# Kernel tuning notes

Hardware: AMD Instinct MI355X
Metric: run time of the kernel (lower is better)

The kernel has to match this reference:

```python
import jax, jax.numpy as jnp
import numpy as np
from jax import lax

NUM_AGNN_LAYERS = 32  # module stacks hidden_dim AGNNConv layers
EPS = 1e-12           # F.normalize clamp


def setup_inputs() -> dict:
    key = jax.random.key(0)
    k1, k2, k3, k4 = jax.random.split(key, 4)
    N, F_in, H, C, E = 100000, 512, 32, 40, 3200000
    x = jax.random.normal(k1, (N, F_in), dtype=jnp.float32)
    edge_index = jax.random.randint(k2, (2, E), 0, N, dtype=jnp.int64)
    W1 = jax.random.normal(k3, (F_in, H), dtype=jnp.float32) * (1.0 / np.sqrt(F_in))
    b1 = jnp.zeros((H,), dtype=jnp.float32)
    W2 = jax.random.normal(k4, (H, C), dtype=jnp.float32) * (1.0 / np.sqrt(H))
    b2 = jnp.zeros((C,), dtype=jnp.float32)
    return {"x": x, "edge_index": edge_index, "W1": W1, "b1": b1, "W2": W2, "b2": b2}


def reference(x, edge_index, W1, b1, W2, b2):
    N = x.shape[0]
    loops = jnp.arange(N, dtype=edge_index.dtype)
    src = jnp.concatenate([edge_index[0], loops])  # message source j
    dst = jnp.concatenate([edge_index[1], loops])  # message target i (softmax group)

    def agnn(h, _):
        # cosine attention, beta = 1 (requires_grad=False)
        norm = jnp.maximum(jnp.linalg.norm(h, axis=-1, keepdims=True), EPS)
        hn = h / norm
        alpha = jnp.sum(hn[src] * hn[dst], axis=-1)               # [E+N]
        m = jax.ops.segment_max(alpha, dst, num_segments=N)       # stable softmax
        e = jnp.exp(alpha - m[dst])
        s = jax.ops.segment_sum(e, dst, num_segments=N)
        coef = e / s[dst]
        out = jax.ops.segment_sum(h[src] * coef[:, None], dst, num_segments=N)
        return out, None

    h = jax.nn.relu(x @ W1 + b1)
    h, _ = lax.scan(agnn, h, None, length=NUM_AGNN_LAYERS)
    logits = h @ W2 + b2
    return jax.nn.log_softmax(logits, axis=1)
```

## Files before the change

kernel.cpp:

```cpp
#include <hip/hip_runtime.h>
#include <math.h>


#define HDIM 32
#define NBMAX 1024
#define BSH 7
#define CHUNK 32768
#define TXP 36
#define TWP 36

typedef _Float16 f16;
typedef _Float16 v2h __attribute__((ext_vector_type(2)));

struct __attribute__((aligned(16))) H8 { v2h p[4]; };
struct __attribute__((aligned(8)))  H4 { v2h p[2]; };

#if defined(__has_builtin)
#if __has_builtin(__builtin_amdgcn_fdot2)
#define FDOT2(a, b, c) __builtin_amdgcn_fdot2((a), (b), (c), false)
#endif
#if __has_builtin(__builtin_amdgcn_update_dpp)
#define HAS_DPP 1
#endif
#endif
#ifndef FDOT2
#define FDOT2(a, b, c) fmaf((float)(a)[1], (float)(b)[1], fmaf((float)(a)[0], (float)(b)[0], (c)))
#endif

static __device__ __forceinline__ float quad_sum(float x) {
#ifdef HAS_DPP
    x += __int_as_float(__builtin_amdgcn_update_dpp(
        0, __float_as_int(x), 0xB1 , 0xF, 0xF, true));
    x += __int_as_float(__builtin_amdgcn_update_dpp(
        0, __float_as_int(x), 0x4E , 0xF, 0xF, true));
#else
    x += __shfl_xor(x, 1);
    x += __shfl_xor(x, 2);
#endif
    return x;
}

static __device__ __forceinline__ int eread(const int* __restrict__ e, int i64, long long idx) {
    return i64 ? e[2 * idx] : e[idx];
}

__global__ void k_flag(const int* __restrict__ e, int* __restrict__ flag) {
    if (blockIdx.x == 0 && threadIdx.x == 0) {
        int z = 0;
        for (int k = 0; k < 64; ++k) z |= e[2 * k + 1];
        *flag = (z == 0) ? 1 : 0;
    }
}

__global__ void k_zero(int* __restrict__ p, int n) {
    int i = blockIdx.x * blockDim.x + threadIdx.x;
    if (i < n) p[i] = 0;
}

__launch_bounds__(256) __global__
void k_hist(const int* __restrict__ e, const int* __restrict__ flag,
            int* __restrict__ gc, int* __restrict__ blockOffs,
            long long E, long long M) {
    __shared__ int bh[NBMAX];
    for (int t = threadIdx.x; t < NBMAX; t += 256) bh[t] = 0;
    __syncthreads();
    int i64 = *flag;
    long long base = (long long)blockIdx.x * CHUNK;
    long long end = base + CHUNK < M ? base + CHUNK : M;
    for (long long m = base + threadIdx.x; m < end; m += 256) {
        int d = (m < E) ? eread(e, i64, E + m) : (int)(m - E);
        atomicAdd(&bh[d >> BSH], 1);
    }
    __syncthreads();
    for (int t = threadIdx.x; t < NBMAX; t += 256) {
        int c = bh[t];
        int off = 0;
        if (c) off = atomicAdd(&gc[t], c);
        blockOffs[(size_t)blockIdx.x * NBMAX + t] = off;
    }
}

__launch_bounds__(256) __global__
void k_bscan(const int* __restrict__ gc, int* __restrict__ bbase,
             int* __restrict__ rp, int N) {
    __shared__ int lds[256];
    int t = threadIdx.x;
    int v[4];
#pragma unroll
    for (int d = 0; d < 4; ++d) v[d] = gc[t * 4 + d];
    int tsum = v[0] + v[1] + v[2] + v[3];
    lds[t] = tsum;
    __syncthreads();
    int acc = tsum;
    for (int sh = 1; sh < 256; sh <<= 1) {
        int x = (t >= sh) ? lds[t - sh] : 0;
        __syncthreads();
        acc += x;
        lds[t] = acc;
        __syncthreads();
    }
    if (t == 255) { rp[N] = acc; bbase[NBMAX] = acc; }
    int run = acc - tsum;
#pragma unroll
    for (int d = 0; d < 4; ++d) { bbase[t * 4 + d] = run; run += v[d]; }
}

__launch_bounds__(256) __global__
void k_part(const int* __restrict__ e, const int* __restrict__ flag,
            const int* __restrict__ bbase, const int* __restrict__ blockOffs,
            int2* __restrict__ pair, long long E, long long M) {
    __shared__ int cur[NBMAX];
    for (int t = threadIdx.x; t < NBMAX; t += 256)
        cur[t] = bbase[t] + blockOffs[(size_t)blockIdx.x * NBMAX + t];
    __syncthreads();
    int i64 = *flag;
    long long base = (long long)blockIdx.x * CHUNK;
    long long end = base + CHUNK < M ? base + CHUNK : M;
    for (long long m = base + threadIdx.x; m < end; m += 256) {
        int s, d;
        if (m < E) { s = eread(e, i64, m); d = eread(e, i64, E + m); }
        else { s = d = (int)(m - E); }
        int pos = atomicAdd(&cur[d >> BSH], 1);
        pair[pos] = make_int2(s, d);
    }
}

__launch_bounds__(256) __global__
void k_fine(const int2* __restrict__ pair, const int* __restrict__ bbase,
            int* __restrict__ rp, int* __restrict__ col, int N) {
    __shared__ int cnt[128];
    __shared__ int sc[128];
    int b = blockIdx.x;
    int beg = bbase[b];
    int end = bbase[b + 1];
    int t = threadIdx.x;
    if (t < 128) cnt[t] = 0;
    __syncthreads();
    for (int k = beg + t; k < end; k += 256)
        atomicAdd(&cnt[pair[k].y & 127], 1);
    __syncthreads();
    if (t < 128) sc[t] = cnt[t];
    __syncthreads();
    for (int sh = 1; sh < 128; sh <<= 1) {
        int x = 0;
        if (t < 128 && t >= sh) x = sc[t - sh];
        __syncthreads();
        if (t < 128) sc[t] += x;
        __syncthreads();
    }
    if (t < 128) {
        int basepos = beg + sc[t] - cnt[t];
        int d = (b << BSH) + t;
        if (d < N) rp[d] = basepos;
        cnt[t] = basepos;
    }
    __syncthreads();
    for (int k = beg + t; k < end; k += 256) {
        int2 p = pair[k];
        int pos = atomicAdd(&cnt[p.y & 127], 1);
        col[pos] = p.x;
    }
}

__launch_bounds__(256, 4) __global__
void k_gemm1(const float* __restrict__ x, const float* __restrict__ W1,
             const float* __restrict__ b1, f16* __restrict__ h, int N) {
    __shared__ float xt[2][128 * TXP];
    __shared__ float wt[2][32 * TWP];
    int tid = threadIdx.x;
    int cg = tid & 7;
    int ty = tid >> 3;
    int rbase = blockIdx.x * 128;
    float4 bias = *(const float4*)(b1 + 4 * cg);
    float acc[4][4];
#pragma unroll
    for (int m = 0; m < 4; ++m) {
        acc[m][0] = bias.x; acc[m][1] = bias.y;
        acc[m][2] = bias.z; acc[m][3] = bias.w;
    }
    int xrow = tid >> 3;
    int xkin = tid & 7;
    float4 gx[4];
    float4 gw;
    {
        int kc = 0;
#pragma unroll
        for (int j = 0; j < 4; ++j) {
            int slot = tid + j * 256;
            int row = slot >> 3, kin = slot & 7;
            int r = rbase + row;
            gx[j] = (r < N) ? *(const float4*)(x + (size_t)r * 512 + kc * 32 + kin * 4)
                            : make_float4(0.f, 0.f, 0.f, 0.f);
        }
        int wrow = tid >> 3, wkin = tid & 7;
        gw = *(const float4*)(W1 + (size_t)(kc * 32 + wrow) * 32 + wkin * 4);
#pragma unroll
        for (int j = 0; j < 4; ++j) {
            int slot = tid + j * 256;
            int row = slot >> 3, kin = slot & 7;
            *(float4*)(&xt[0][row * TXP + kin * 4]) = gx[j];
        }
        *(float4*)(&wt[0][wrow * TWP + wkin * 4]) = gw;
    }
    __syncthreads();
    for (int kc = 0; kc < 16; ++kc) {
        int buf = kc & 1;
        if (kc + 1 < 16) {
            int kn = kc + 1;
#pragma unroll
            for (int j = 0; j < 4; ++j) {
                int slot = tid + j * 256;
                int row = slot >> 3, kin = slot & 7;
                int r = rbase + row;
                gx[j] = (r < N) ? *(const float4*)(x + (size_t)r * 512 + kn * 32 + kin * 4)
                                : make_float4(0.f, 0.f, 0.f, 0.f);
            }
            gw = *(const float4*)(W1 + (size_t)(kn * 32 + (tid >> 3)) * 32 + (tid & 7) * 4);
        }
        const float* xb = xt[buf];
        const float* wb = wt[buf];
#pragma unroll
        for (int k4 = 0; k4 < 8; ++k4) {
            float4 w0 = *(const float4*)(wb + (k4 * 4 + 0) * TWP + 4 * cg);
            float4 w1 = *(const float4*)(wb + (k4 * 4 + 1) * TWP + 4 * cg);
            float4 w2 = *(const float4*)(wb + (k4 * 4 + 2) * TWP + 4 * cg);
            float4 w3 = *(const float4*)(wb + (k4 * 4 + 3) * TWP + 4 * cg);
#pragma unroll
            for (int m = 0; m < 4; ++m) {
                float4 xv = *(const float4*)(xb + (ty + 32 * m) * TXP + k4 * 4);
                acc[m][0] = fmaf(xv.x, w0.x, acc[m][0]);
                acc[m][1] = fmaf(xv.x, w0.y, acc[m][1]);
                acc[m][2] = fmaf(xv.x, w0.z, acc[m][2]);
                acc[m][3] = fmaf(xv.x, w0.w, acc[m][3]);
                acc[m][0] = fmaf(xv.y, w1.x, acc[m][0]);
                acc[m][1] = fmaf(xv.y, w1.y, acc[m][1]);
                acc[m][2] = fmaf(xv.y, w1.z, acc[m][2]);
                acc[m][3] = fmaf(xv.y, w1.w, acc[m][3]);
                acc[m][0] = fmaf(xv.z, w2.x, acc[m][0]);
                acc[m][1] = fmaf(xv.z, w2.y, acc[m][1]);
                acc[m][2] = fmaf(xv.z, w2.z, acc[m][2]);
                acc[m][3] = fmaf(xv.z, w2.w, acc[m][3]);
                acc[m][0] = fmaf(xv.w, w3.x, acc[m][0]);
                acc[m][1] = fmaf(xv.w, w3.y, acc[m][1]);
                acc[m][2] = fmaf(xv.w, w3.z, acc[m][2]);
                acc[m][3] = fmaf(xv.w, w3.w, acc[m][3]);
            }
        }
        if (kc + 1 < 16) {
            int nbuf = buf ^ 1;
#pragma unroll
            for (int j = 0; j < 4; ++j) {
                int slot = tid + j * 256;
                int row = slot >> 3, kin = slot & 7;
                *(float4*)(&xt[nbuf][row * TXP + kin * 4]) = gx[j];
            }
            *(float4*)(&wt[nbuf][(tid >> 3) * TWP + (tid & 7) * 4]) = gw;
            __syncthreads();
        }
    }
    (void)xrow; (void)xkin;
#pragma unroll
    for (int m = 0; m < 4; ++m) {
        int r = rbase + ty + 32 * m;
        if (r < N) {
            H4 o;
            o.p[0][0] = (f16)fmaxf(acc[m][0], 0.0f);
            o.p[0][1] = (f16)fmaxf(acc[m][1], 0.0f);
            o.p[1][0] = (f16)fmaxf(acc[m][2], 0.0f);
            o.p[1][1] = (f16)fmaxf(acc[m][3], 0.0f);
            *(H4*)(h + (size_t)r * HDIM + 4 * cg) = o;
        }
    }
}

__launch_bounds__(256) __global__
void k_agnn(const f16* __restrict__ h_in, f16* __restrict__ h_out,
            const int* __restrict__ rp, const int* __restrict__ col, int N) {
    int wave = threadIdx.x >> 6;
    int lane = threadIdx.x & 63;
    int i = blockIdx.x * 4 + wave;
    if (i >= N) return;
    int beg = rp[i];
    int deg = rp[i + 1] - beg;
    int eloc = lane >> 2;
    int c8 = lane & 3;
    H8 hi = *(const H8*)(h_in + (size_t)i * HDIM + 8 * c8);
    float dsi = 0.0f;
#pragma unroll
    for (int j = 0; j < 4; ++j) dsi = FDOT2(hi.p[j], hi.p[j], dsi);
    dsi = quad_sum(dsi);
    float inv_i = 1.0f / fmaxf(sqrtf(dsi), 1e-12f);
    float s_run = 0.0f;
    float acc[8] = {0.f, 0.f, 0.f, 0.f, 0.f, 0.f, 0.f, 0.f};
    int nchunk = (deg + 15) >> 4;
    int cv = (lane < deg) ? col[beg + lane] : 0;
    H8 rA, rB;
    bool vA, vB = false;
    {
        vA = eloc < deg;
        int s = __shfl(cv, eloc);
        s = vA ? s : 0;
        rA = *(const H8*)(h_in + (size_t)s * HDIM + 8 * c8);
    }
    if (nchunk > 1) {
        int idx = 16 + eloc;
        vB = idx < deg;
        int s = __shfl(cv, 16 | eloc);
        s = vB ? s : 0;
        rB = *(const H8*)(h_in + (size_t)s * HDIM + 8 * c8);
    } else {
        rB = hi;
    }
    for (int ck = 0; ck < nchunk; ++ck) {
        H8 rc = rA;
        bool vc = vA;
        rA = rB; vA = vB;
        int nc = ck + 2;
        if (nc < nchunk) {
            if ((nc & 3) == 0) {
                int idx64 = nc * 16 + lane;
                cv = (idx64 < deg) ? col[beg + idx64] : 0;
            }
            int idx = nc * 16 + eloc;
            vB = idx < deg;
            int s = __shfl(cv, ((nc & 3) << 4) | eloc);
            s = vB ? s : 0;
            rB = *(const H8*)(h_in + (size_t)s * HDIM + 8 * c8);
        }
        float dot = 0.0f, dsj = 0.0f;
#pragma unroll
        for (int j = 0; j < 4; ++j) {
            dot = FDOT2(rc.p[j], hi.p[j], dot);
            dsj = FDOT2(rc.p[j], rc.p[j], dsj);
        }
        dot = quad_sum(dot);
        dsj = quad_sum(dsj);
        float inv_j = 1.0f / fmaxf(sqrtf(dsj), 1e-12f);
        float e = vc ? __expf(fmaf(dot, inv_i * inv_j, -1.0f)) : 0.0f;
        s_run += e;
#pragma unroll
        for (int j = 0; j < 4; ++j) {
            acc[2 * j + 0] = fmaf(e, (float)rc.p[j][0], acc[2 * j + 0]);
            acc[2 * j + 1] = fmaf(e, (float)rc.p[j][1], acc[2 * j + 1]);
        }
    }
    float s_tot = s_run;
#pragma unroll
    for (int mask = 4; mask <= 32; mask <<= 1) s_tot += __shfl_xor(s_tot, mask);
#pragma unroll
    for (int mask = 4; mask <= 32; mask <<= 1) {
#pragma unroll
        for (int j = 0; j < 8; ++j) acc[j] += __shfl_xor(acc[j], mask);
    }
    float invs = 1.0f / s_tot;
#pragma unroll
    for (int j = 0; j < 8; ++j) acc[j] *= invs;
    if (lane < 4) {
        H8 o;
#pragma unroll
        for (int j = 0; j < 4; ++j) {
            o.p[j][0] = (f16)acc[2 * j + 0];
            o.p[j][1] = (f16)acc[2 * j + 1];
        }
        *(H8*)(h_out + (size_t)i * HDIM + 8 * lane) = o;
    }
}

__launch_bounds__(256) __global__
void k_gemm2(const f16* __restrict__ h, const float* __restrict__ W2,
             const float* __restrict__ b2, float* __restrict__ out, int N) {
    int wave = threadIdx.x >> 6;
    int lane = threadIdx.x & 63;
    int i = blockIdx.x * 4 + wave;
    if (i >= N) return;
    bool act = lane < 40;
    float acc = act ? b2[lane] : 0.0f;
    const f16* hr = h + (size_t)i * HDIM;
#pragma unroll
    for (int k = 0; k < HDIM; ++k) {
        float hk = (float)hr[k];
        float w = act ? W2[k * 40 + lane] : 0.0f;
        acc = fmaf(hk, w, acc);
    }
    float logit = act ? acc : -INFINITY;
    float m = logit;
#pragma unroll
    for (int mask = 32; mask >= 1; mask >>= 1) m = fmaxf(m, __shfl_xor(m, mask));
    float e = act ? __expf(logit - m) : 0.0f;
    float s = e;
#pragma unroll
    for (int mask = 32; mask >= 1; mask >>= 1) s += __shfl_xor(s, mask);
    float res = logit - m - __logf(s);
    if (act) out[(size_t)i * 40 + lane] = res;
}

extern "C" void kernel_launch(void* const* d_in, const int* in_sizes, int n_in,
                              void* d_out, int out_size, void* d_ws, size_t ws_size,
                              hipStream_t stream) {
    const float* x  = (const float*)d_in[0];
    const int*   e  = (const int*)d_in[1];
    const float* W1 = (const float*)d_in[2];
    const float* b1 = (const float*)d_in[3];
    const float* W2 = (const float*)d_in[4];
    const float* b2 = (const float*)d_in[5];
    float* out = (float*)d_out;

    const long long E = (long long)in_sizes[1] / 2;
    const int N = in_sizes[0] / 512;
    const long long M = E + N;
    const int nblk = (int)((M + CHUNK - 1) / CHUNK);

    char* w = (char*)d_ws;
    auto alloc = [&](size_t bytes) -> void* {
        void* p = (void*)w;
        w += (bytes + 255) & ~(size_t)255;
        return p;
    };
    int*  flag      = (int*)alloc(4);
    int*  gc        = (int*)alloc(NBMAX * 4);
    int*  bbase     = (int*)alloc((NBMAX + 1) * 4);
    int*  blockOffs = (int*)alloc((size_t)nblk * NBMAX * 4);
    int2* pair      = (int2*)alloc((size_t)M * 8);
    int*  rp        = (int*)alloc(((size_t)N + 1) * 4);
    int*  col       = (int*)alloc((size_t)M * 4);
    f16*  hA   = (f16*)alloc((size_t)N * HDIM * 2);
    f16*  hB   = (f16*)alloc((size_t)N * HDIM * 2);
    if ((size_t)(w - (char*)d_ws) > ws_size) return;

    k_flag<<<1, 64, 0, stream>>>(e, flag);
    k_zero<<<(NBMAX + 255) / 256, 256, 0, stream>>>(gc, NBMAX);
    k_hist<<<nblk, 256, 0, stream>>>(e, flag, gc, blockOffs, E, M);
    k_bscan<<<1, 256, 0, stream>>>(gc, bbase, rp, N);
    k_part<<<nblk, 256, 0, stream>>>(e, flag, bbase, blockOffs, pair, E, M);
    k_fine<<<NBMAX, 256, 0, stream>>>(pair, bbase, rp, col, N);

    k_gemm1<<<(N + 127) / 128, 256, 0, stream>>>(x, W1, b1, hA, N);

    f16 *hin = hA, *hout = hB;
    for (int l = 0; l < 32; ++l) {
        k_agnn<<<(N + 3) / 4, 256, 0, stream>>>(hin, hout, rp, col, N);
        f16* t = hin; hin = hout; hout = t;
    }
    k_gemm2<<<(N + 3) / 4, 256, 0, stream>>>(hin, W2, b2, out, N);
}
```

Before: 2.231 ms.

## Precompute per-node inverse norms in producer kernels and deepen gather prefetch to four chunks

Each producer kernel (gemm1 and every AGNN layer) now writes a per-node inverse L2 norm next to the fp16 features. This removes the per-edge norm computation (an extra dot product, a quad reduction and a sqrt/reciprocal) from the AGNN inner loop, at the cost of one extra 4-byte gather per edge. The neighbour loop is also restructured so four chunks of column indices and rows are loaded ahead instead of two, raising memory-level parallelism. Norms are now computed from fp32 values before the fp16 rounding, so they differ slightly from norms of the stored fp16 features.

Result: no change. 2.256 ms (+1.1%).

```diff
diff --git a/kernel.cpp b/kernel.cpp
--- a/kernel.cpp
+++ b/kernel.cpp
@@ -164,7 +164,8 @@
 
 __launch_bounds__(256, 4) __global__
 void k_gemm1(const float* __restrict__ x, const float* __restrict__ W1,
-             const float* __restrict__ b1, f16* __restrict__ h, int N) {
+             const float* __restrict__ b1, f16* __restrict__ h,
+             float* __restrict__ invn, int N) {
     __shared__ float xt[2][128 * TXP];
     __shared__ float wt[2][32 * TWP];
     int tid = threadIdx.x;
@@ -178,8 +179,6 @@
         acc[m][0] = bias.x; acc[m][1] = bias.y;
         acc[m][2] = bias.z; acc[m][3] = bias.w;
     }
-    int xrow = tid >> 3;
-    int xkin = tid & 7;
     float4 gx[4];
     float4 gw;
     {
@@ -258,23 +257,32 @@
             __syncthreads();
         }
     }
-    (void)xrow; (void)xkin;
 #pragma unroll
     for (int m = 0; m < 4; ++m) {
         int r = rbase + ty + 32 * m;
+        float hv[4];
+        float ss = 0.0f;
+#pragma unroll
+        for (int j = 0; j < 4; ++j) {
+            hv[j] = fmaxf(acc[m][j], 0.0f);
+            ss = fmaf(hv[j], hv[j], ss);
+        }
+        ss += __shfl_xor(ss, 1);
+        ss += __shfl_xor(ss, 2);
+        ss += __shfl_xor(ss, 4);
         if (r < N) {
             H4 o;
-            o.p[0][0] = (f16)fmaxf(acc[m][0], 0.0f);
-            o.p[0][1] = (f16)fmaxf(acc[m][1], 0.0f);
-            o.p[1][0] = (f16)fmaxf(acc[m][2], 0.0f);
-            o.p[1][1] = (f16)fmaxf(acc[m][3], 0.0f);
+            o.p[0][0] = (f16)hv[0]; o.p[0][1] = (f16)hv[1];
+            o.p[1][0] = (f16)hv[2]; o.p[1][1] = (f16)hv[3];
             *(H4*)(h + (size_t)r * HDIM + 4 * cg) = o;
-        }
-    }
-}
-
-__launch_bounds__(256) __global__
-void k_agnn(const f16* __restrict__ h_in, f16* __restrict__ h_out,
+            if (cg == 0) invn[r] = 1.0f / fmaxf(sqrtf(ss), 1e-12f);
+        }
+    }
+}
+
+__launch_bounds__(256) __global__
+void k_agnn(const f16* __restrict__ h_in, const float* __restrict__ inv_in,
+            f16* __restrict__ h_out, float* __restrict__ inv_out,
             const int* __restrict__ rp, const int* __restrict__ col, int N) {
     int wave = threadIdx.x >> 6;
     int lane = threadIdx.x & 63;
@@ -284,66 +292,68 @@
     int deg = rp[i + 1] - beg;
     int eloc = lane >> 2;
     int c8 = lane & 3;
+    float inv_i = inv_in[i];
     H8 hi = *(const H8*)(h_in + (size_t)i * HDIM + 8 * c8);
-    float dsi = 0.0f;
-#pragma unroll
-    for (int j = 0; j < 4; ++j) dsi = FDOT2(hi.p[j], hi.p[j], dsi);
-    dsi = quad_sum(dsi);
-    float inv_i = 1.0f / fmaxf(sqrtf(dsi), 1e-12f);
     float s_run = 0.0f;
     float acc[8] = {0.f, 0.f, 0.f, 0.f, 0.f, 0.f, 0.f, 0.f};
     int nchunk = (deg + 15) >> 4;
-    int cv = (lane < deg) ? col[beg + lane] : 0;
-    H8 rA, rB;
-    bool vA, vB = false;
-    {
-        vA = eloc < deg;
-        int s = __shfl(cv, eloc);
-        s = vA ? s : 0;
-        rA = *(const H8*)(h_in + (size_t)s * HDIM + 8 * c8);
-    }
-    if (nchunk > 1) {
-        int idx = 16 + eloc;
-        vB = idx < deg;
-        int s = __shfl(cv, 16 | eloc);
-        s = vB ? s : 0;
-        rB = *(const H8*)(h_in + (size_t)s * HDIM + 8 * c8);
-    } else {
-        rB = hi;
-    }
-    for (int ck = 0; ck < nchunk; ++ck) {
-        H8 rc = rA;
-        bool vc = vA;
-        rA = rB; vA = vB;
-        int nc = ck + 2;
-        if (nc < nchunk) {
-            if ((nc & 3) == 0) {
-                int idx64 = nc * 16 + lane;
-                cv = (idx64 < deg) ? col[beg + idx64] : 0;
-            }
-            int idx = nc * 16 + eloc;
-            vB = idx < deg;
-            int s = __shfl(cv, ((nc & 3) << 4) | eloc);
-            s = vB ? s : 0;
-            rB = *(const H8*)(h_in + (size_t)s * HDIM + 8 * c8);
-        }
-        float dot = 0.0f, dsj = 0.0f;
-#pragma unroll
-        for (int j = 0; j < 4; ++j) {
-            dot = FDOT2(rc.p[j], hi.p[j], dot);
-            dsj = FDOT2(rc.p[j], rc.p[j], dsj);
-        }
-        dot = quad_sum(dot);
-        dsj = quad_sum(dsj);
-        float inv_j = 1.0f / fmaxf(sqrtf(dsj), 1e-12f);
-        float e = vc ? __expf(fmaf(dot, inv_i * inv_j, -1.0f)) : 0.0f;
-        s_run += e;
-#pragma unroll
-        for (int j = 0; j < 4; ++j) {
-            acc[2 * j + 0] = fmaf(e, (float)rc.p[j][0], acc[2 * j + 0]);
-            acc[2 * j + 1] = fmaf(e, (float)rc.p[j][1], acc[2 * j + 1]);
-        }
-    }
+
+#define CLOADK(k) ((16 * (k) + eloc) < deg ? col[beg + 16 * (k) + eloc] : 0)
+#define RLOAD(Rv, iv, s) do { \
+        Rv = *(const H8*)(h_in + (size_t)(s) * HDIM + 8 * c8); \
+        iv = inv_in[(s)]; \
+    } while (0)
+#define PROC(Rv, iv, vf) do { \
+        float dot_ = 0.0f; \
+        _Pragma("unroll") \
+        for (int j_ = 0; j_ < 4; ++j_) dot_ = FDOT2(Rv.p[j_], hi.p[j_], dot_); \
+        dot_ = quad_sum(dot_); \
+        float e_ = (vf) ? __expf(fmaf(dot_, inv_i * (iv), -1.0f)) : 0.0f; \
+        s_run += e_; \
+        _Pragma("unroll") \
+        for (int j_ = 0; j_ < 4; ++j_) { \
+            acc[2 * j_ + 0] = fmaf(e_, (float)Rv.p[j_][0], acc[2 * j_ + 0]); \
+            acc[2 * j_ + 1] = fmaf(e_, (float)Rv.p[j_][1], acc[2 * j_ + 1]); \
+        } \
+    } while (0)
+
+    int c0 = CLOADK(0), c1 = CLOADK(1), c2 = CLOADK(2), c3 = CLOADK(3);
+    bool v0 = (eloc) < deg;
+    bool v1 = (16 + eloc) < deg;
+    bool v2 = (32 + eloc) < deg;
+    bool v3 = (48 + eloc) < deg;
+    H8 R0, R1, R2, R3;
+    float i0, i1, i2, i3;
+    RLOAD(R0, i0, c0);
+    RLOAD(R1, i1, c1);
+    RLOAD(R2, i2, c2);
+    RLOAD(R3, i3, c3);
+    int n0 = 0, n1 = 0, n2 = 0, n3 = 0;
+    if (nchunk > 4) { n0 = CLOADK(4); n1 = CLOADK(5); n2 = CLOADK(6); n3 = CLOADK(7); }
+
+    int g = 0;
+    if (nchunk > 4) {
+        while (true) {
+            PROC(R0, i0, v0); v0 = (16 * (g + 4) + eloc) < deg; RLOAD(R0, i0, n0);
+            PROC(R1, i1, v1); v1 = (16 * (g + 5) + eloc) < deg; RLOAD(R1, i1, n1);
+            PROC(R2, i2, v2); v2 = (16 * (g + 6) + eloc) < deg; RLOAD(R2, i2, n2);
+            PROC(R3, i3, v3); v3 = (16 * (g + 7) + eloc) < deg; RLOAD(R3, i3, n3);
+            g += 4;
+            if (g + 4 >= nchunk) break;
+            n0 = CLOADK(g + 4); n1 = CLOADK(g + 5);
+            n2 = CLOADK(g + 6); n3 = CLOADK(g + 7);
+        }
+    }
+    int rem = nchunk - g;
+    PROC(R0, i0, v0);
+    if (rem > 1) PROC(R1, i1, v1);
+    if (rem > 2) PROC(R2, i2, v2);
+    if (rem > 3) PROC(R3, i3, v3);
+
+#undef CLOADK
+#undef RLOAD
+#undef PROC
+
     float s_tot = s_run;
 #pragma unroll
     for (int mask = 4; mask <= 32; mask <<= 1) s_tot += __shfl_xor(s_tot, mask);
@@ -353,8 +363,13 @@
         for (int j = 0; j < 8; ++j) acc[j] += __shfl_xor(acc[j], mask);
     }
     float invs = 1.0f / s_tot;
-#pragma unroll
-    for (int j = 0; j < 8; ++j) acc[j] *= invs;
+    float ss = 0.0f;
+#pragma unroll
+    for (int j = 0; j < 8; ++j) {
+        acc[j] *= invs;
+        ss = fmaf(acc[j], acc[j], ss);
+    }
+    ss = quad_sum(ss);
     if (lane < 4) {
         H8 o;
 #pragma unroll
@@ -363,6 +378,7 @@
             o.p[j][1] = (f16)acc[2 * j + 1];
         }
         *(H8*)(h_out + (size_t)i * HDIM + 8 * lane) = o;
+        if (lane == 0) inv_out[i] = 1.0f / fmaxf(sqrtf(ss), 1e-12f);
     }
 }
 
@@ -425,6 +441,8 @@
     int*  col       = (int*)alloc((size_t)M * 4);
     f16*  hA   = (f16*)alloc((size_t)N * HDIM * 2);
     f16*  hB   = (f16*)alloc((size_t)N * HDIM * 2);
+    float* invA = (float*)alloc((size_t)N * 4);
+    float* invB = (float*)alloc((size_t)N * 4);
     if ((size_t)(w - (char*)d_ws) > ws_size) return;
 
     k_flag<<<1, 64, 0, stream>>>(e, flag);
@@ -434,12 +452,14 @@
     k_part<<<nblk, 256, 0, stream>>>(e, flag, bbase, blockOffs, pair, E, M);
     k_fine<<<NBMAX, 256, 0, stream>>>(pair, bbase, rp, col, N);
 
-    k_gemm1<<<(N + 127) / 128, 256, 0, stream>>>(x, W1, b1, hA, N);
+    k_gemm1<<<(N + 127) / 128, 256, 0, stream>>>(x, W1, b1, hA, invA, N);
 
     f16 *hin = hA, *hout = hB;
+    float *iin = invA, *iout = invB;
     for (int l = 0; l < 32; ++l) {
-        k_agnn<<<(N + 3) / 4, 256, 0, stream>>>(hin, hout, rp, col, N);
+        k_agnn<<<(N + 3) / 4, 256, 0, stream>>>(hin, iin, hout, iout, rp, col, N);
         f16* t = hin; hin = hout; hout = t;
+        float* ti = iin; iin = iout; iout = ti;
     }
     k_gemm2<<<(N + 3) / 4, 256, 0, stream>>>(hin, W2, b2, out, N);
 }
```
